# Performance work log

Measured on AMD Instinct MI355X. Metric: run time of the kernel, lower is better.

The kernel has to match this reference:

```python
import jax, jax.numpy as jnp
import numpy as np

B, L, D = 2, 2048, 2048
NUM_HEADS = 32
KV_GROUPS = 8
GROUP_SIZE = NUM_HEADS // KV_GROUPS  # 4
HEAD_DIM = D // NUM_HEADS            # 64


def _rope_tables(L, hd):
    # standard RoPE angle tables, duplicated across halves to width hd
    inv_freq = 1.0 / (10000.0 ** (np.arange(0, hd, 2, dtype=np.float32) / hd))
    ang = np.arange(L, dtype=np.float32)[:, None] * inv_freq[None, :]  # [L, hd/2]
    cos = np.concatenate([np.cos(ang), np.cos(ang)], axis=-1)
    sin = np.concatenate([np.sin(ang), np.sin(ang)], axis=-1)
    return jnp.asarray(cos), jnp.asarray(sin)


def setup_inputs() -> dict:
    key = jax.random.key(0)
    ks = jax.random.split(key, 6)
    x = jax.random.normal(ks[0], (B, L, D), dtype=jnp.float32)
    mask = jnp.triu(jnp.ones((L, L), dtype=bool), k=1)  # causal: True above diag
    cos, sin = _rope_tables(L, HEAD_DIM)
    s = 0.02
    Wq = jax.random.normal(ks[1], (D, D), dtype=jnp.float32) * s
    Wk = jax.random.normal(ks[2], (D, KV_GROUPS * HEAD_DIM), dtype=jnp.float32) * s
    Wv = jax.random.normal(ks[3], (D, KV_GROUPS * HEAD_DIM), dtype=jnp.float32) * s
    Wo = jax.random.normal(ks[4], (D, D), dtype=jnp.float32) * s
    bo = jnp.zeros((D,), dtype=jnp.float32)
    return {"x": x, "mask": mask, "cos": cos, "sin": sin,
            "Wq": Wq, "Wk": Wk, "Wv": Wv, "Wo": Wo, "bo": bo}


def _apply_rope(t, cos, sin):
    # t: [B, H, L, hd]
    hd = t.shape[-1]
    t1, t2 = t[..., : hd // 2], t[..., hd // 2:]
    rotated = jnp.concatenate([-t2, t1], axis=-1)
    return t * cos[None, None, :, :] + rotated * sin[None, None, :, :]


def reference(x, mask, cos, sin, Wq, Wk, Wv, Wo, bo):
    Bv, Lv, Dv = x.shape
    hd = HEAD_DIM
    q = (x @ Wq).reshape(Bv, Lv, NUM_HEADS, hd).transpose(0, 2, 1, 3)   # [B,H,L,hd]
    k = (x @ Wk).reshape(Bv, Lv, KV_GROUPS, hd).transpose(0, 2, 1, 3)   # [B,G,L,hd]
    v = (x @ Wv).reshape(Bv, Lv, KV_GROUPS, hd).transpose(0, 2, 1, 3)
    q = _apply_rope(q, cos, sin)
    k = _apply_rope(k, cos, sin)
    k = jnp.repeat(k, GROUP_SIZE, axis=1)  # [B,H,L,hd]
    v = jnp.repeat(v, GROUP_SIZE, axis=1)
    scores = jnp.einsum('bhqd,bhkd->bhqk', q, k) / jnp.sqrt(jnp.float32(hd))
    scores = jnp.where(mask[None, None, :, :], -jnp.inf, scores)
    attn = jax.nn.softmax(scores, axis=-1)
    out = jnp.einsum('bhqk,bhkd->bhqd', attn, v)         # [B,H,L,hd]
    out = out.transpose(0, 2, 1, 3).reshape(Bv, Lv, Dv)  # [B,L,D]
    return out @ Wo + bo
```

## Files before the change

### kernel.cpp

```cpp
#include <hip/hip_runtime.h>
#include <cstdint>

typedef unsigned short UST;
typedef __bf16 v8bf __attribute__((ext_vector_type(8)));
typedef float v4f __attribute__((ext_vector_type(4)));

static __device__ __forceinline__ UST f2b(float f) {
  union { float f; uint32_t u; } c; c.f = f;
  uint32_t u = c.u;
  u += 0x7fffu + ((u >> 16) & 1u);
  return (UST)(u >> 16);
}
static __device__ __forceinline__ float b2f(UST h) {
  union { uint32_t u; float f; } c; c.u = ((uint32_t)h) << 16;
  return c.f;
}
static __device__ __forceinline__ uint32_t cvtpk(float lo, float hi) {
  uint32_t r;
  asm("v_cvt_pk_bf16_f32 %0, %1, %2" : "=v"(r) : "v"(lo), "v"(hi));
  return r;
}
static __device__ __forceinline__ float fexp2(float x) {
  float r;
  asm("v_exp_f32 %0, %1" : "=v"(r) : "v"(x));
  return r;
}
template <int N>
static __device__ __forceinline__ void wait_vm() {
  asm volatile("s_waitcnt vmcnt(%0)" :: "i"(N));
}

static __device__ __forceinline__ void gl_lds16(const UST* g, UST* l) {
  __builtin_amdgcn_global_load_lds(
      (const __attribute__((address_space(1))) void*)g,
      (__attribute__((address_space(3))) void*)l, 16, 0, 0);
}

__global__ __launch_bounds__(256) void k_cast(const float* __restrict__ src,
                                              UST* __restrict__ dst) {
  size_t i = (size_t)blockIdx.x * 256 + threadIdx.x;
  const float4* s4 = reinterpret_cast<const float4*>(src) + 2 * i;
  float4 a = s4[0], b = s4[1];
  union { UST s[8]; uint4 v; } r;
  r.s[0] = f2b(a.x); r.s[1] = f2b(a.y); r.s[2] = f2b(a.z); r.s[3] = f2b(a.w);
  r.s[4] = f2b(b.x); r.s[5] = f2b(b.y); r.s[6] = f2b(b.z); r.s[7] = f2b(b.w);
  reinterpret_cast<uint4*>(dst)[i] = r.v;
}

__global__ __launch_bounds__(256) void k_castT(const float* __restrict__ W,
                                               UST* __restrict__ dst, int N, int K) {
  __shared__ float tile[32][33];
  int nt = blockIdx.x * 32, kt = blockIdx.y * 32;
  int tx = threadIdx.x, ty = threadIdx.y;
#pragma unroll
  for (int r = 0; r < 4; ++r)
    tile[ty + r * 8][tx] = W[(size_t)(kt + ty + r * 8) * N + nt + tx];
  __syncthreads();
#pragma unroll
  for (int r = 0; r < 4; ++r)
    dst[(size_t)(nt + ty + r * 8) * K + kt + tx] = f2b(tile[tx][ty + r * 8]);
}

template <int BM, int BN, int WM, int WN, int NMH, int EPI>
__global__ __launch_bounds__(512, 2) void k_gemm2(const UST* __restrict__ A,
                                                  const UST* __restrict__ Bt,
                                                  void* __restrict__ Cv,
                                                  const float* __restrict__ bias,
                                                  int M, int N, int K, int ntn) {
  constexpr int WMR = BM / WM, WNR = BN / WN;
  constexpr int MF = WMR / 16, NF = WNR / 16, MH = MF / NMH;
  constexpr int CA = BM / 128;
  constexpr int CBF = BN / 128;
  constexpr int BREM = (BN % 128) / 64;
  constexpr int AELEMS = 4 * BM * 32;
  __shared__ __align__(16) UST lds[AELEMS + 4 * BN * 32];

  int tid = threadIdx.x, w = tid >> 6, lane = tid & 63;
  int lr = lane & 15, lg = lane >> 4;
  int wm = w / WN, wn = w % WN;

  int q = (int)gridDim.x >> 3;
  int bid = (int)blockIdx.x;
  int swz = (bid & 7) * q + (bid >> 3);
  int mBlk = (swz / ntn) * BM, nBlk = (swz % ntn) * BN;

  v4f acc[MF][NF];
#pragma unroll
  for (int i = 0; i < MF; ++i)
#pragma unroll
    for (int j = 0; j < NF; ++j) acc[i][j] = (v4f){0.f, 0.f, 0.f, 0.f};

  int srow = tid >> 2, scol = (tid & 3) * 8;
  const UST* Abase = A + (size_t)(mBlk + srow) * K + scol;
  const UST* Bbase = Bt + (size_t)(nBlk + srow) * K + scol;
  int ldsW = w * 512;

  auto stageA = [&](int buf, int s, int kt) {
#pragma unroll
    for (int i = 0; i < CA; ++i)
      gl_lds16(Abase + (size_t)(i * 128) * K + kt * 64 + s * 32,
               &lds[(buf * 2 + s) * BM * 32 + i * 4096 + ldsW]);
  };
  auto stageB = [&](int buf, int s, int kt) {
#pragma unroll
    for (int i = 0; i < CBF; ++i)
      gl_lds16(Bbase + (size_t)(i * 128) * K + kt * 64 + s * 32,
               &lds[AELEMS + (buf * 2 + s) * BN * 32 + i * 4096 + ldsW]);
    if constexpr (BREM) {
      if (w < 4)
        gl_lds16(Bbase + (size_t)(CBF * 128) * K + kt * 64 + s * 32,
                 &lds[AELEMS + (buf * 2 + s) * BN * 32 + CBF * 4096 + ldsW]);
    }
  };
  auto waitNK = [&]() {
    if constexpr (BREM) {
      if (w < 4) wait_vm<CA + CBF + 1>();
      else       wait_vm<CA + CBF>();
    } else {
      wait_vm<CA + CBF>();
    }
  };
  auto ldA = [&](int buf, int s, int f) -> v8bf {
    int row = wm * WMR + f * 16 + lr;
    return *(const v8bf*)&lds[((buf * 2 + s) * BM + row) * 32 + lg * 8];
  };
  auto ldB = [&](int buf, int s, int nf) -> v8bf {
    int row = wn * WNR + nf * 16 + lr;
    return *(const v8bf*)&lds[AELEMS + ((buf * 2 + s) * BN + row) * 32 + lg * 8];
  };

  int NT = K >> 6;
  stageA(0, 0, 0); stageB(0, 0, 0); stageA(0, 1, 0); stageB(0, 1, 0);
  waitNK();
  __builtin_amdgcn_s_barrier();

  for (int kt = 0; kt < NT; ++kt) {
    int buf = kt & 1, nb = buf ^ 1;
    bool more = (kt + 1 < NT);
#pragma unroll
    for (int s = 0; s < 2; ++s) {
      v8bf bfr[NF];
#pragma unroll
      for (int mh = 0; mh < NMH; ++mh) {
        v8bf afr[MH];
        if (mh == 0) {
#pragma unroll
          for (int nf = 0; nf < NF; ++nf) bfr[nf] = ldB(buf, s, nf);
        }
#pragma unroll
        for (int f = 0; f < MH; ++f) afr[f] = ldA(buf, s, mh * MH + f);
        if constexpr (NMH == 2) {
          if (mh == 0) {
            if (more) stageA(nb, s, kt + 1);
          } else {
            if (more) { stageB(nb, s, kt + 1); waitNK(); }
            else if (s == 0) wait_vm<0>();
          }
        } else {
          if (more) { stageA(nb, s, kt + 1); stageB(nb, s, kt + 1); waitNK(); }
          else if (s == 0) wait_vm<0>();
        }
        __builtin_amdgcn_s_barrier();
        __builtin_amdgcn_s_setprio(1);
#pragma unroll
        for (int f = 0; f < MH; ++f)
#pragma unroll
          for (int nf = 0; nf < NF; ++nf)
            acc[mh * MH + f][nf] = __builtin_amdgcn_mfma_f32_16x16x32_bf16(
                afr[f], bfr[nf], acc[mh * MH + f][nf], 0, 0, 0);
        __builtin_amdgcn_s_setprio(0);
        __builtin_amdgcn_s_barrier();
      }
    }
  }

  int row0 = mBlk + wm * WMR + lg * 4;
  int col0 = nBlk + wn * WNR + lr;
#pragma unroll
  for (int fm = 0; fm < MF; ++fm)
#pragma unroll
    for (int nf = 0; nf < NF; ++nf)
#pragma unroll
      for (int r = 0; r < 4; ++r) {
        int row = row0 + fm * 16 + r;
        int col = col0 + nf * 16;
        if constexpr (EPI == 0) {
          ((UST*)Cv)[(size_t)row * N + col] = f2b(acc[fm][nf][r]);
        } else {
          ((float*)Cv)[(size_t)row * N + col] = acc[fm][nf][r] + bias[col];
        }
      }
}

__global__ __launch_bounds__(256) void k_rope(const UST* __restrict__ qkv,
                                              const float* __restrict__ cosT,
                                              const float* __restrict__ sinT,
                                              UST* __restrict__ qh,
                                              UST* __restrict__ kh) {
  int idx = blockIdx.x * 256 + threadIdx.x;
  int d = idx & 31;
  int hh = (idx >> 5) % 40;
  int row = idx / 1280;
  int l = row & 2047, b = row >> 11;
  int col = (hh < 32) ? hh * 64 : 2048 + (hh - 32) * 64;
  float t1 = b2f(qkv[(size_t)row * 3072 + col + d]);
  float t2 = b2f(qkv[(size_t)row * 3072 + col + d + 32]);
  float c = cosT[l * 64 + d], s = sinT[l * 64 + d];
  float o1 = t1 * c - t2 * s;
  float o2 = t2 * c + t1 * s;
  if (hh < 32) {
    size_t base = (((size_t)b * 32 + hh) * 2048 + l) * 64 + d;
    qh[base] = f2b(o1 * 0.125f);
    qh[base + 32] = f2b(o2 * 0.125f);
  } else {
    size_t base = (((size_t)b * 8 + (hh - 32)) * 2048 + l) * 64 + d;
    kh[base] = f2b(o1);
    kh[base + 32] = f2b(o2);
  }
}

__global__ __launch_bounds__(256) void k_vtrans(const UST* __restrict__ qkv,
                                                UST* __restrict__ vt) {
  __shared__ __align__(16) UST tl[64][72];
  int lt = blockIdx.x, bg = blockIdx.y;
  int b = bg >> 3, g = bg & 7;
  int t = threadIdx.x;
  int li = t >> 2, d0 = (t & 3) * 16;
  const UST* src = qkv + (size_t)(b * 2048 + lt * 64 + li) * 3072 + 2560 + g * 64 + d0;
  *(uint4*)&tl[li][d0] = *(const uint4*)src;
  *(uint4*)&tl[li][d0 + 8] = *(const uint4*)(src + 8);
  __syncthreads();
  int d = t >> 2, l0 = (t & 3) * 16;
  union { UST u[8]; uint4 v; } r0, r1;
#pragma unroll
  for (int e = 0; e < 8; ++e) r0.u[e] = tl[l0 + e][d];
#pragma unroll
  for (int e = 0; e < 8; ++e) r1.u[e] = tl[l0 + 8 + e][d];
  UST* dstp = vt + (size_t)((b * 8 + g) * 64 + d) * 2048 + (size_t)lt * 64 + l0;
  *(uint4*)dstp = r0.v;
  *(uint4*)(dstp + 8) = r1.v;
}

__global__ __launch_bounds__(512, 4) void k_attn(const UST* __restrict__ qh,
                                                 const UST* __restrict__ kh,
                                                 const UST* __restrict__ vt,
                                                 UST* __restrict__ outp) {
  __shared__ __align__(16) UST k_s[128 * 72];
  __shared__ __align__(16) UST v_s[64 * 136];
  __shared__ __align__(16) UST p_s[8][16 * 136];
  int bx = blockIdx.x, h = blockIdx.y, b = blockIdx.z;
  int g = h >> 2;
  int tid = threadIdx.x, w = tid >> 6, lane = tid & 63;
  int lr = lane & 15, lg = lane >> 4;

  int ksr = tid >> 2, ksc = (tid & 3) * 16;
  int vsr = tid >> 3, vsc = (tid & 7) * 16;
  const UST* kbase = kh + ((size_t)(b * 8 + g) * 2048 + ksr) * 64 + ksc;
  const UST* vbase = vt + ((size_t)(b * 8 + g) * 64 + vsr) * 2048 + vsc;
  UST* kdst = &k_s[ksr * 72 + ksc];
  UST* vdst = &v_s[vsr * 136 + vsc];

  for (int half = 0; half < 2; ++half) {
    int qt = half ? (15 - bx) : bx;
    int qbase = qt * 128 + w * 16;

    const UST* qp = qh + ((size_t)(b * 32 + h) * 2048 + qbase + lr) * 64 + lg * 8;
    v8bf qf0 = *(const v8bf*)qp;
    v8bf qf1 = *(const v8bf*)(qp + 32);

    float m = -1e30f, ls = 0.f;
    v4f o[4];
#pragma unroll
    for (int dt = 0; dt < 4; ++dt) o[dt] = (v4f){0.f, 0.f, 0.f, 0.f};

    __syncthreads();
    uint4 pk0 = *(const uint4*)kbase, pk1 = *(const uint4*)(kbase + 8);
    uint4 pv0 = *(const uint4*)vbase, pv1 = *(const uint4*)(vbase + 8);
    *(uint4*)kdst = pk0; *(uint4*)(kdst + 8) = pk1;
    *(uint4*)vdst = pv0; *(uint4*)(vdst + 8) = pv1;

    for (int j = 0; j <= qt; ++j) {
      __syncthreads();
      bool pref = (j < qt);
      if (pref) {
        const UST* kg = kbase + (size_t)(j + 1) * 8192;
        const UST* vg = vbase + (j + 1) * 128;
        pk0 = *(const uint4*)kg; pk1 = *(const uint4*)(kg + 8);
        pv0 = *(const uint4*)vg; pv1 = *(const uint4*)(vg + 8);
      }

      v4f st[8];
      __builtin_amdgcn_s_setprio(1);
#pragma unroll
      for (int kt = 0; kt < 8; ++kt) {
        const UST* kr = &k_s[(kt * 16 + lr) * 72 + lg * 8];
        v8bf kf0 = *(const v8bf*)kr;
        v8bf kf1 = *(const v8bf*)(kr + 32);
        v4f z = (v4f){0.f, 0.f, 0.f, 0.f};
        z = __builtin_amdgcn_mfma_f32_16x16x32_bf16(kf0, qf0, z, 0, 0, 0);
        z = __builtin_amdgcn_mfma_f32_16x16x32_bf16(kf1, qf1, z, 0, 0, 0);
        st[kt] = z;
      }
      __builtin_amdgcn_s_setprio(0);
      if (j == qt) {
        int qg = qbase + lr;
#pragma unroll
        for (int kt = 0; kt < 8; ++kt)
#pragma unroll
          for (int r = 0; r < 4; ++r) {
            int kg2 = j * 128 + kt * 16 + 4 * lg + r;
            if (kg2 > qg) st[kt][r] = -1e30f;
          }
      }

      float t0 = fmaxf(fmaxf(st[0][0], st[0][1]), fmaxf(st[0][2], st[0][3]));
      float t1 = fmaxf(fmaxf(st[1][0], st[1][1]), fmaxf(st[1][2], st[1][3]));
      float t2 = fmaxf(fmaxf(st[2][0], st[2][1]), fmaxf(st[2][2], st[2][3]));
      float t3 = fmaxf(fmaxf(st[3][0], st[3][1]), fmaxf(st[3][2], st[3][3]));
      float t4 = fmaxf(fmaxf(st[4][0], st[4][1]), fmaxf(st[4][2], st[4][3]));
      float t5 = fmaxf(fmaxf(st[5][0], st[5][1]), fmaxf(st[5][2], st[5][3]));
      float t6 = fmaxf(fmaxf(st[6][0], st[6][1]), fmaxf(st[6][2], st[6][3]));
      float t7 = fmaxf(fmaxf(st[7][0], st[7][1]), fmaxf(st[7][2], st[7][3]));
      float mx = fmaxf(fmaxf(fmaxf(t0, t1), fmaxf(t2, t3)),
                       fmaxf(fmaxf(t4, t5), fmaxf(t6, t7)));
      mx = fmaxf(mx, __shfl_xor(mx, 16));
      mx = fmaxf(mx, __shfl_xor(mx, 32));

      if (!__all(mx <= m + 8.f)) {
        float mn = fmaxf(m, mx);
        float al = __expf(m - mn);
        m = mn;
        ls *= al;
#pragma unroll
        for (int r = 0; r < 4; ++r) {
          float ar = __shfl(al, 4 * lg + r);
          o[0][r] *= ar; o[1][r] *= ar; o[2][r] *= ar; o[3][r] *= ar;
        }
      }

      constexpr float LOG2E = 1.44269504f;
      float mlog = m * LOG2E;
      float rs = 0.f;
      UST* pw = &p_s[w][lr * 136 + 4 * lg];
#pragma unroll
      for (int kt = 0; kt < 8; ++kt) {
        float p0 = fexp2(__builtin_fmaf(st[kt][0], LOG2E, -mlog));
        float p1 = fexp2(__builtin_fmaf(st[kt][1], LOG2E, -mlog));
        float p2 = fexp2(__builtin_fmaf(st[kt][2], LOG2E, -mlog));
        float p3 = fexp2(__builtin_fmaf(st[kt][3], LOG2E, -mlog));
        rs += (p0 + p1) + (p2 + p3);
        uint2 q2;
        q2.x = cvtpk(p0, p1);
        q2.y = cvtpk(p2, p3);
        *(uint2*)(pw + kt * 16) = q2;
      }
      rs += __shfl_xor(rs, 16);
      rs += __shfl_xor(rs, 32);
      ls += rs;

      __builtin_amdgcn_s_setprio(1);
#pragma unroll
      for (int kk = 0; kk < 4; ++kk) {
        v8bf pa = *(const v8bf*)&p_s[w][lr * 136 + kk * 32 + lg * 8];
#pragma unroll
        for (int dt = 0; dt < 4; ++dt) {
          v8bf vb = *(const v8bf*)&v_s[(dt * 16 + lr) * 136 + kk * 32 + lg * 8];
          o[dt] = __builtin_amdgcn_mfma_f32_16x16x32_bf16(pa, vb, o[dt], 0, 0, 0);
        }
      }
      __builtin_amdgcn_s_setprio(0);

      __syncthreads();
      if (pref) {
        *(uint4*)kdst = pk0; *(uint4*)(kdst + 8) = pk1;
        *(uint4*)vdst = pv0; *(uint4*)(vdst + 8) = pv1;
      }
    }

    float iv = 1.f / ls;
#pragma unroll
    for (int r = 0; r < 4; ++r) {
      float ivr = __shfl(iv, 4 * lg + r);
      size_t rowb = ((size_t)b * 2048 + qbase + 4 * lg + r) * 2048 + h * 64 + lr;
#pragma unroll
      for (int dt = 0; dt < 4; ++dt)
        outp[rowb + dt * 16] = f2b(o[dt][r] * ivr);
    }
  }
}

extern "C" void kernel_launch(void* const* d_in, const int* in_sizes, int n_in,
                              void* d_out, int out_size, void* d_ws, size_t ws_size,
                              hipStream_t stream) {
  const float* x    = (const float*)d_in[0];
  const float* cosT = (const float*)d_in[2];
  const float* sinT = (const float*)d_in[3];
  const float* Wq   = (const float*)d_in[4];
  const float* Wk   = (const float*)d_in[5];
  const float* Wv   = (const float*)d_in[6];
  const float* Wo   = (const float*)d_in[7];
  const float* bo   = (const float*)d_in[8];
  float* out = (float*)d_out;

  char* ws = (char*)d_ws;
  UST* xb   = (UST*)(ws);
  UST* wcat = (UST*)(ws + 16777216);
  UST* wot  = (UST*)(ws + 29360128);
  UST* qkv  = (UST*)(ws + 37748736);
  UST* qhp  = (UST*)(ws + 62914560);
  UST* khp  = (UST*)(ws + 79691776);
  UST* vtp  = (UST*)(ws + 83886080);
  UST* attn_o = xb;

  k_cast<<<4096, 256, 0, stream>>>(x, xb);
  k_castT<<<dim3(64, 64), dim3(32, 8), 0, stream>>>(Wq, wcat, 2048, 2048);
  k_castT<<<dim3(16, 64), dim3(32, 8), 0, stream>>>(Wk, wcat + (size_t)2048 * 2048, 512, 2048);
  k_castT<<<dim3(16, 64), dim3(32, 8), 0, stream>>>(Wv, wcat + (size_t)2560 * 2048, 512, 2048);
  k_castT<<<dim3(64, 64), dim3(32, 8), 0, stream>>>(Wo, wot, 2048, 2048);

  k_gemm2<256, 192, 2, 4, 2, 0><<<256, 512, 0, stream>>>(xb, wcat, qkv, nullptr,
                                                         4096, 3072, 2048, 16);
  k_rope<<<20480, 256, 0, stream>>>(qkv, cosT, sinT, qhp, khp);
  k_vtrans<<<dim3(32, 16), 256, 0, stream>>>(qkv, vtp);
  k_attn<<<dim3(8, 32, 2), 512, 0, stream>>>(qhp, khp, vtp, attn_o);
  k_gemm2<256, 128, 4, 2, 1, 1><<<256, 512, 0, stream>>>(attn_o, wot, out, bo,
                                                         4096, 2048, 2048, 16);
}
```

Before: 206.1 us.

## Split causal attention per q-tile, XOR-swizzle LDS, and interleave softmax with PV

Result: slower. 363.1 us (+76.2%).

```diff
diff --git a/kernel.cpp b/kernel.cpp
--- a/kernel.cpp
+++ b/kernel.cpp
@@ -241,109 +241,115 @@
   *(uint4*)(dstp + 8) = r1.v;
 }
 
-__global__ __launch_bounds__(512, 4) void k_attn(const UST* __restrict__ qh,
+__global__ __launch_bounds__(512, 6) void k_attn(const UST* __restrict__ qh,
                                                  const UST* __restrict__ kh,
                                                  const UST* __restrict__ vt,
                                                  UST* __restrict__ outp) {
-  __shared__ __align__(16) UST k_s[128 * 72];
-  __shared__ __align__(16) UST v_s[64 * 136];
-  __shared__ __align__(16) UST p_s[8][16 * 136];
-  int bx = blockIdx.x, h = blockIdx.y, b = blockIdx.z;
+  __shared__ __align__(16) UST k_s[128 * 64];
+  __shared__ __align__(16) UST v_s[64 * 128];
+  __shared__ __align__(16) UST p_s[8 * 16 * 64];
+  int qt = 15 - (int)blockIdx.x;
+  int h = blockIdx.y, b = blockIdx.z;
   int g = h >> 2;
   int tid = threadIdx.x, w = tid >> 6, lane = tid & 63;
   int lr = lane & 15, lg = lane >> 4;
+  int lsw = (lr & 7) << 3;
+  int qbase = qt * 128 + w * 16;
+
+  const UST* qp = qh + ((size_t)(b * 32 + h) * 2048 + qbase + lr) * 64 + lg * 8;
+  v8bf qf0 = *(const v8bf*)qp;
+  v8bf qf1 = *(const v8bf*)(qp + 32);
+
+  float m = -1e30f, ls = 0.f;
+  v4f o[4];
+#pragma unroll
+  for (int dt = 0; dt < 4; ++dt) o[dt] = (v4f){0.f, 0.f, 0.f, 0.f};
 
   int ksr = tid >> 2, ksc = (tid & 3) * 16;
   int vsr = tid >> 3, vsc = (tid & 7) * 16;
   const UST* kbase = kh + ((size_t)(b * 8 + g) * 2048 + ksr) * 64 + ksc;
   const UST* vbase = vt + ((size_t)(b * 8 + g) * 64 + vsr) * 2048 + vsc;
-  UST* kdst = &k_s[ksr * 72 + ksc];
-  UST* vdst = &v_s[vsr * 136 + vsc];
-
-  for (int half = 0; half < 2; ++half) {
-    int qt = half ? (15 - bx) : bx;
-    int qbase = qt * 128 + w * 16;
-
-    const UST* qp = qh + ((size_t)(b * 32 + h) * 2048 + qbase + lr) * 64 + lg * 8;
-    v8bf qf0 = *(const v8bf*)qp;
-    v8bf qf1 = *(const v8bf*)(qp + 32);
-
-    float m = -1e30f, ls = 0.f;
-    v4f o[4];
-#pragma unroll
-    for (int dt = 0; dt < 4; ++dt) o[dt] = (v4f){0.f, 0.f, 0.f, 0.f};
-
+  int ksz = (ksr & 7) << 3, vsz = (vsr & 7) << 3;
+  UST* kd0 = &k_s[ksr * 64 + (ksc ^ ksz)];
+  UST* kd1 = &k_s[ksr * 64 + ((ksc + 8) ^ ksz)];
+  UST* vd0 = &v_s[vsr * 128 + (vsc ^ vsz)];
+  UST* vd1 = &v_s[vsr * 128 + ((vsc + 8) ^ vsz)];
+
+  {
+    uint4 a0 = *(const uint4*)kbase, a1 = *(const uint4*)(kbase + 8);
+    uint4 b0 = *(const uint4*)vbase, b1 = *(const uint4*)(vbase + 8);
+    *(uint4*)kd0 = a0; *(uint4*)kd1 = a1;
+    *(uint4*)vd0 = b0; *(uint4*)vd1 = b1;
+  }
+
+  UST* pwb = &p_s[w * 1024 + lr * 64];
+
+  for (int j = 0; j <= qt; ++j) {
     __syncthreads();
-    uint4 pk0 = *(const uint4*)kbase, pk1 = *(const uint4*)(kbase + 8);
-    uint4 pv0 = *(const uint4*)vbase, pv1 = *(const uint4*)(vbase + 8);
-    *(uint4*)kdst = pk0; *(uint4*)(kdst + 8) = pk1;
-    *(uint4*)vdst = pv0; *(uint4*)(vdst + 8) = pv1;
-
-    for (int j = 0; j <= qt; ++j) {
-      __syncthreads();
-      bool pref = (j < qt);
-      if (pref) {
-        const UST* kg = kbase + (size_t)(j + 1) * 8192;
-        const UST* vg = vbase + (j + 1) * 128;
-        pk0 = *(const uint4*)kg; pk1 = *(const uint4*)(kg + 8);
-        pv0 = *(const uint4*)vg; pv1 = *(const uint4*)(vg + 8);
-      }
-
-      v4f st[8];
-      __builtin_amdgcn_s_setprio(1);
-#pragma unroll
-      for (int kt = 0; kt < 8; ++kt) {
-        const UST* kr = &k_s[(kt * 16 + lr) * 72 + lg * 8];
-        v8bf kf0 = *(const v8bf*)kr;
-        v8bf kf1 = *(const v8bf*)(kr + 32);
-        v4f z = (v4f){0.f, 0.f, 0.f, 0.f};
-        z = __builtin_amdgcn_mfma_f32_16x16x32_bf16(kf0, qf0, z, 0, 0, 0);
-        z = __builtin_amdgcn_mfma_f32_16x16x32_bf16(kf1, qf1, z, 0, 0, 0);
-        st[kt] = z;
-      }
-      __builtin_amdgcn_s_setprio(0);
-      if (j == qt) {
-        int qg = qbase + lr;
-#pragma unroll
-        for (int kt = 0; kt < 8; ++kt)
-#pragma unroll
-          for (int r = 0; r < 4; ++r) {
-            int kg2 = j * 128 + kt * 16 + 4 * lg + r;
-            if (kg2 > qg) st[kt][r] = -1e30f;
-          }
-      }
-
-      float t0 = fmaxf(fmaxf(st[0][0], st[0][1]), fmaxf(st[0][2], st[0][3]));
-      float t1 = fmaxf(fmaxf(st[1][0], st[1][1]), fmaxf(st[1][2], st[1][3]));
-      float t2 = fmaxf(fmaxf(st[2][0], st[2][1]), fmaxf(st[2][2], st[2][3]));
-      float t3 = fmaxf(fmaxf(st[3][0], st[3][1]), fmaxf(st[3][2], st[3][3]));
-      float t4 = fmaxf(fmaxf(st[4][0], st[4][1]), fmaxf(st[4][2], st[4][3]));
-      float t5 = fmaxf(fmaxf(st[5][0], st[5][1]), fmaxf(st[5][2], st[5][3]));
-      float t6 = fmaxf(fmaxf(st[6][0], st[6][1]), fmaxf(st[6][2], st[6][3]));
-      float t7 = fmaxf(fmaxf(st[7][0], st[7][1]), fmaxf(st[7][2], st[7][3]));
-      float mx = fmaxf(fmaxf(fmaxf(t0, t1), fmaxf(t2, t3)),
-                       fmaxf(fmaxf(t4, t5), fmaxf(t6, t7)));
-      mx = fmaxf(mx, __shfl_xor(mx, 16));
-      mx = fmaxf(mx, __shfl_xor(mx, 32));
-
-      if (!__all(mx <= m + 8.f)) {
-        float mn = fmaxf(m, mx);
-        float al = __expf(m - mn);
-        m = mn;
-        ls *= al;
+    bool pref = (j < qt);
+    uint4 pk0, pk1, pv0, pv1;
+    if (pref) {
+      const UST* kg = kbase + (size_t)(j + 1) * 8192;
+      pk0 = *(const uint4*)kg; pk1 = *(const uint4*)(kg + 8);
+    }
+
+    v4f st[8];
+    __builtin_amdgcn_s_setprio(1);
+#pragma unroll
+    for (int kt = 0; kt < 8; ++kt) {
+      const UST* krow = &k_s[(kt * 16 + lr) * 64];
+      v8bf kf0 = *(const v8bf*)&krow[(lg * 8) ^ lsw];
+      v8bf kf1 = *(const v8bf*)&krow[(32 + lg * 8) ^ lsw];
+      v4f z = (v4f){0.f, 0.f, 0.f, 0.f};
+      z = __builtin_amdgcn_mfma_f32_16x16x32_bf16(kf0, qf0, z, 0, 0, 0);
+      z = __builtin_amdgcn_mfma_f32_16x16x32_bf16(kf1, qf1, z, 0, 0, 0);
+      st[kt] = z;
+    }
+    __builtin_amdgcn_s_setprio(0);
+    if (j == qt) {
+      int qg = qbase + lr;
+#pragma unroll
+      for (int kt = 0; kt < 8; ++kt)
 #pragma unroll
         for (int r = 0; r < 4; ++r) {
-          float ar = __shfl(al, 4 * lg + r);
-          o[0][r] *= ar; o[1][r] *= ar; o[2][r] *= ar; o[3][r] *= ar;
+          int kp = j * 128 + kt * 16 + 4 * lg + r;
+          if (kp > qg) st[kt][r] = -1e30f;
         }
-      }
-
-      constexpr float LOG2E = 1.44269504f;
-      float mlog = m * LOG2E;
-      float rs = 0.f;
-      UST* pw = &p_s[w][lr * 136 + 4 * lg];
-#pragma unroll
-      for (int kt = 0; kt < 8; ++kt) {
+    }
+
+    float t0 = fmaxf(fmaxf(st[0][0], st[0][1]), fmaxf(st[0][2], st[0][3]));
+    float t1 = fmaxf(fmaxf(st[1][0], st[1][1]), fmaxf(st[1][2], st[1][3]));
+    float t2 = fmaxf(fmaxf(st[2][0], st[2][1]), fmaxf(st[2][2], st[2][3]));
+    float t3 = fmaxf(fmaxf(st[3][0], st[3][1]), fmaxf(st[3][2], st[3][3]));
+    float t4 = fmaxf(fmaxf(st[4][0], st[4][1]), fmaxf(st[4][2], st[4][3]));
+    float t5 = fmaxf(fmaxf(st[5][0], st[5][1]), fmaxf(st[5][2], st[5][3]));
+    float t6 = fmaxf(fmaxf(st[6][0], st[6][1]), fmaxf(st[6][2], st[6][3]));
+    float t7 = fmaxf(fmaxf(st[7][0], st[7][1]), fmaxf(st[7][2], st[7][3]));
+    float mx = fmaxf(fmaxf(fmaxf(t0, t1), fmaxf(t2, t3)),
+                     fmaxf(fmaxf(t4, t5), fmaxf(t6, t7)));
+    mx = fmaxf(mx, __shfl_xor(mx, 16));
+    mx = fmaxf(mx, __shfl_xor(mx, 32));
+
+    if (!__all(mx <= m + 8.f)) {
+      float mn = fmaxf(m, mx);
+      float al = __expf(m - mn);
+      m = mn;
+      ls *= al;
+#pragma unroll
+      for (int r = 0; r < 4; ++r) {
+        float ar = __shfl(al, 4 * lg + r);
+        o[0][r] *= ar; o[1][r] *= ar; o[2][r] *= ar; o[3][r] *= ar;
+      }
+    }
+
+    constexpr float LOG2E = 1.44269504f;
+    float mlog = m * LOG2E;
+    float rs = 0.f;
+#pragma unroll
+    for (int c = 0; c < 2; ++c) {
+#pragma unroll
+      for (int k2 = 0; k2 < 4; ++k2) {
+        int kt = c * 4 + k2;
         float p0 = fexp2(__builtin_fmaf(st[kt][0], LOG2E, -mlog));
         float p1 = fexp2(__builtin_fmaf(st[kt][1], LOG2E, -mlog));
         float p2 = fexp2(__builtin_fmaf(st[kt][2], LOG2E, -mlog));
@@ -352,40 +358,44 @@
         uint2 q2;
         q2.x = cvtpk(p0, p1);
         q2.y = cvtpk(p2, p3);
-        *(uint2*)(pw + kt * 16) = q2;
-      }
-      rs += __shfl_xor(rs, 16);
-      rs += __shfl_xor(rs, 32);
-      ls += rs;
-
+        *(uint2*)&pwb[((k2 * 16 + (lg >> 1) * 8) ^ lsw) + (lg & 1) * 4] = q2;
+      }
+      if (c == 0 && pref) {
+        const UST* vg = vbase + (j + 1) * 128;
+        pv0 = *(const uint4*)vg; pv1 = *(const uint4*)(vg + 8);
+      }
       __builtin_amdgcn_s_setprio(1);
 #pragma unroll
-      for (int kk = 0; kk < 4; ++kk) {
-        v8bf pa = *(const v8bf*)&p_s[w][lr * 136 + kk * 32 + lg * 8];
+      for (int kkl = 0; kkl < 2; ++kkl) {
+        int kk = c * 2 + kkl;
+        v8bf pa = *(const v8bf*)&pwb[(kkl * 32 + lg * 8) ^ lsw];
 #pragma unroll
         for (int dt = 0; dt < 4; ++dt) {
-          v8bf vb = *(const v8bf*)&v_s[(dt * 16 + lr) * 136 + kk * 32 + lg * 8];
+          v8bf vb = *(const v8bf*)&v_s[(dt * 16 + lr) * 128 + ((kk * 32 + lg * 8) ^ lsw)];
           o[dt] = __builtin_amdgcn_mfma_f32_16x16x32_bf16(pa, vb, o[dt], 0, 0, 0);
         }
       }
       __builtin_amdgcn_s_setprio(0);
-
-      __syncthreads();
-      if (pref) {
-        *(uint4*)kdst = pk0; *(uint4*)(kdst + 8) = pk1;
-        *(uint4*)vdst = pv0; *(uint4*)(vdst + 8) = pv1;
-      }
-    }
-
-    float iv = 1.f / ls;
-#pragma unroll
-    for (int r = 0; r < 4; ++r) {
-      float ivr = __shfl(iv, 4 * lg + r);
-      size_t rowb = ((size_t)b * 2048 + qbase + 4 * lg + r) * 2048 + h * 64 + lr;
-#pragma unroll
-      for (int dt = 0; dt < 4; ++dt)
-        outp[rowb + dt * 16] = f2b(o[dt][r] * ivr);
-    }
+    }
+    rs += __shfl_xor(rs, 16);
+    rs += __shfl_xor(rs, 32);
+    ls += rs;
+
+    __syncthreads();
+    if (pref) {
+      *(uint4*)kd0 = pk0; *(uint4*)kd1 = pk1;
+      *(uint4*)vd0 = pv0; *(uint4*)vd1 = pv1;
+    }
+  }
+
+  float iv = 1.f / ls;
+#pragma unroll
+  for (int r = 0; r < 4; ++r) {
+    float ivr = __shfl(iv, 4 * lg + r);
+    size_t rowb = ((size_t)b * 2048 + qbase + 4 * lg + r) * 2048 + h * 64 + lr;
+#pragma unroll
+    for (int dt = 0; dt < 4; ++dt)
+      outp[rowb + dt * 16] = f2b(o[dt][r] * ivr);
   }
 }
 
@@ -422,7 +432,7 @@
                                                          4096, 3072, 2048, 16);
   k_rope<<<20480, 256, 0, stream>>>(qkv, cosT, sinT, qhp, khp);
   k_vtrans<<<dim3(32, 16), 256, 0, stream>>>(qkv, vtp);
-  k_attn<<<dim3(8, 32, 2), 512, 0, stream>>>(qhp, khp, vtp, attn_o);
+  k_attn<<<dim3(16, 32, 2), 512, 0, stream>>>(qhp, khp, vtp, attn_o);
   k_gemm2<256, 128, 4, 2, 1, 1><<<256, 512, 0, stream>>>(attn_o, wot, out, bo,
                                                          4096, 2048, 2048, 16);
 }
```
